# Kernel tuning notes

Measured on AMD Instinct MI355X. Metric: run time of the kernel, lower is better.

## Reference

```python
import jax, jax.numpy as jnp
import numpy as np

DIM = 1024
HEADS = 16
HEAD_DIM = DIM // HEADS


def setup_inputs() -> dict:
    key = jax.random.key(0)
    k_x, k_qkv, k_ow, k_ob = jax.random.split(key, 4)
    x = jax.random.normal(k_x, (2, 2048, DIM), dtype=jnp.float32)
    # nn.Linear(dim, 3*dim, bias=False): weight shape [3*dim, dim], y = x @ W.T
    w_qkv = jax.random.normal(k_qkv, (3 * DIM, DIM), dtype=jnp.float32) * (DIM ** -0.5)
    # nn.Linear(dim, dim) with bias
    w_o = jax.random.normal(k_ow, (DIM, DIM), dtype=jnp.float32) * (DIM ** -0.5)
    b_o = jax.random.normal(k_ob, (DIM,), dtype=jnp.float32) * 0.02
    return {"x": x, "w_qkv": w_qkv, "w_o": w_o, "b_o": b_o}


def reference(x, w_qkv, w_o, b_o):
    b, n, _ = x.shape
    scale = DIM ** -0.5  # NOTE: source scales by full dim, not head dim
    # qkv projection: [b, n, 3*dim]
    qkv = jnp.einsum('bnd,ed->bne', x, w_qkv)
    # 'b n (qkv h d) -> qkv b h n d'
    qkv = qkv.reshape(b, n, 3, HEADS, HEAD_DIM)
    q = jnp.transpose(qkv[:, :, 0], (0, 2, 1, 3))  # [b, h, n, d]
    k = jnp.transpose(qkv[:, :, 1], (0, 2, 1, 3))
    v = jnp.transpose(qkv[:, :, 2], (0, 2, 1, 3))
    scores = jnp.einsum('bhqd,bhkd->bhqk', q, k) * scale  # [b, h, n, n]
    attn = jax.nn.softmax(scores, axis=-1)
    out = jnp.einsum('bhqk,bhkd->bhqd', attn, v)  # [b, h, n, d]
    out = jnp.transpose(out, (0, 2, 1, 3)).reshape(b, n, DIM)  # 'b h n d -> b n (h d)'
    out = jnp.einsum('bnd,ed->bne', out, w_o) + b_o
    return out
```

## Files before the change

### kernel.cpp

```cpp
#include <hip/hip_runtime.h>
#include <stdint.h>


#define DIM 1024
#define SEQ 2048
#define BATCH 2
#define ROWS 4096
#define RSTRIDE 3072

typedef __bf16 bf16_t;
typedef bf16_t bf16x4 __attribute__((ext_vector_type(4)));
typedef bf16_t bf16x8 __attribute__((ext_vector_type(8)));
typedef float f32x4 __attribute__((ext_vector_type(4)));

__device__ __forceinline__ ushort f2bf(float f) {
    uint32_t u;
    __builtin_memcpy(&u, &f, 4);
    uint32_t r = (u + 0x7fffu + ((u >> 16) & 1u)) >> 16;
    return (ushort)r;
}

__device__ __forceinline__ void store_out(ushort* p, float v) { *p = f2bf(v); }
__device__ __forceinline__ void store_out(float* p, float v) { *p = v; }

__device__ __forceinline__ void gl_lds16(const void* g, void* l) {
    __builtin_amdgcn_global_load_lds(
        (const __attribute__((address_space(1))) void*)g,
        (__attribute__((address_space(3))) void*)l, 16, 0, 0);
}

__global__ __launch_bounds__(256) void cvt3_kernel(
    const float* __restrict__ x, const float* __restrict__ wq,
    const float* __restrict__ wo, ushort* __restrict__ dst) {
    size_t i = ((size_t)blockIdx.x * 256 + threadIdx.x) * 8;
    const size_t n_x = (size_t)ROWS * DIM;
    const size_t n_wq = (size_t)3 * DIM * DIM;
    const float* src;
    size_t off;
    if (i < n_x) {
        src = x; off = i;
    } else if (i < n_x + n_wq) {
        src = wq; off = i - n_x;
    } else {
        src = wo; off = i - n_x - n_wq;
    }
    float4 a = *(const float4*)(src + off);
    float4 b = *(const float4*)(src + off + 4);
    uint4 u;
    u.x = (uint)f2bf(a.x) | ((uint)f2bf(a.y) << 16);
    u.y = (uint)f2bf(a.z) | ((uint)f2bf(a.w) << 16);
    u.z = (uint)f2bf(b.x) | ((uint)f2bf(b.y) << 16);
    u.w = (uint)f2bf(b.z) | ((uint)f2bf(b.w) << 16);
    *(uint4*)(dst + i) = u;
}

template <typename OutT, int BN>
__global__ __launch_bounds__(256) void gemm_bt_kernel(
    const ushort* __restrict__ A, const ushort* __restrict__ B,
    const float* __restrict__ bias, OutT* __restrict__ C,
    int M, int N, int K) {
    constexpr int JN = BN / 32;
    __shared__ __align__(16) ushort sA[128 * 64];
    __shared__ __align__(16) ushort sB[BN * 64];

    const int tid = threadIdx.x;
    const int lane = tid & 63, w = tid >> 6;
    const int quad = lane >> 4, l15 = lane & 15;
    const int wm = (w >> 1) * 64, wn = (w & 1) * (BN / 2);
    const int bm = blockIdx.y, bn = blockIdx.x;

    f32x4 acc[4][JN];
#pragma unroll
    for (int i = 0; i < 4; i++)
#pragma unroll
        for (int j = 0; j < JN; j++) acc[i][j] = (f32x4){0.f, 0.f, 0.f, 0.f};

    const ushort* Abase = A + (size_t)(bm * 128) * K;
    const ushort* Bbase = B + (size_t)(bn * BN) * K;
    const int rd = lane >> 3, c8 = lane & 7;
    const int sw = l15 & 7;

    for (int kk = 0; kk < K; kk += 64) {
        __syncthreads();
#pragma unroll
        for (int t = 0; t < 4; t++) {
            int row = w * 32 + t * 8;
            gl_lds16(Abase + (size_t)(row + rd) * K + kk + ((c8 ^ rd) * 8),
                     sA + row * 64);
        }
#pragma unroll
        for (int t = 0; t < BN / 32; t++) {
            int row = w * 8 + t * 32;
            gl_lds16(Bbase + (size_t)(row + rd) * K + kk + ((c8 ^ rd) * 8),
                     sB + row * 64);
        }
        __syncthreads();

#pragma unroll
        for (int kh = 0; kh < 2; kh++) {
            bf16x8 af[4], bfr[JN];
#pragma unroll
            for (int i = 0; i < 4; i++)
                af[i] = *(const bf16x8*)((const bf16_t*)sA +
                        (wm + i * 16 + l15) * 64 + (((kh * 4 + quad) ^ sw) * 8));
#pragma unroll
            for (int j = 0; j < JN; j++)
                bfr[j] = *(const bf16x8*)((const bf16_t*)sB +
                        (wn + j * 16 + l15) * 64 + (((kh * 4 + quad) ^ sw) * 8));
#pragma unroll
            for (int i = 0; i < 4; i++)
#pragma unroll
                for (int j = 0; j < JN; j++)
                    acc[i][j] = __builtin_amdgcn_mfma_f32_16x16x32_bf16(
                        af[i], bfr[j], acc[i][j], 0, 0, 0);
        }
    }

#pragma unroll
    for (int i = 0; i < 4; i++)
#pragma unroll
        for (int j = 0; j < JN; j++) {
            int col = bn * BN + wn + j * 16 + l15;
            float bv = bias ? bias[col] : 0.f;
#pragma unroll
            for (int r = 0; r < 4; r++) {
                int row = bm * 128 + wm + i * 16 + quad * 4 + r;
                store_out(&C[(size_t)row * N + col], acc[i][j][r] + bv);
            }
        }
}

__global__ __launch_bounds__(512) void flash_attn_kernel(
    const ushort* __restrict__ qkv, ushort* __restrict__ out) {
    __shared__ __align__(16) ushort sK[128 * 64];
    __shared__ __align__(16) ushort sVt[64 * 128];
    __shared__ __align__(16) ushort sP[128 * 64];

    const int tid = threadIdx.x;
    const int lane = tid & 63, w = tid >> 6;
    const int quad = lane >> 4, l15 = lane & 15;
    const int sw = l15 & 7;
    const int bh = blockIdx.y, b = bh >> 4, h = bh & 15;
    const int q0 = blockIdx.x * 128;
    const ushort* qkvb = qkv + (size_t)b * SEQ * RSTRIDE + h * 64;

    const ushort* qrow = qkvb + (size_t)(q0 + w * 16 + l15) * RSTRIDE;
    const bf16x8 aq0 = *(const bf16x8*)(qrow + quad * 8);
    const bf16x8 aq1 = *(const bf16x8*)(qrow + 32 + quad * 8);

    const int krow = tid >> 3, kc8 = tid & 7;
    const int kdst = krow * 64 + ((kc8 ^ (krow & 7)) * 8);
    const int vrp = tid & 63, vc = tid >> 6;
    const int vch = vrp >> 2, vlo = vrp & 3;

    uint4 kreg0, kreg1, va, vb;
    {
        const ushort* kp0 = qkvb + (size_t)krow * RSTRIDE + DIM + kc8 * 8;
        kreg0 = *(const uint4*)kp0;
        kreg1 = *(const uint4*)(kp0 + (size_t)64 * RSTRIDE);
        const ushort* v0 = qkvb + (size_t)(2 * vrp) * RSTRIDE + 2 * DIM + vc * 8;
        va = *(const uint4*)v0;
        vb = *(const uint4*)(v0 + RSTRIDE);
    }

    f32x4 l_acc = (f32x4){0.f, 0.f, 0.f, 0.f};
    f32x4 o[4];
#pragma unroll
    for (int j = 0; j < 4; j++) o[j] = (f32x4){0.f, 0.f, 0.f, 0.f};

    bf16x8 vones;
#pragma unroll
    for (int e = 0; e < 8; e++) vones[e] = (bf16_t)1.0f;

    const float c_exp = 0.04508422f;

    uint* vt32 = (uint*)sVt;
    bf16_t* sPb = (bf16_t*)sP;
    const int swp = (l15 & 7) ^ (((l15 >> 3) & 1) << 1);
    for (int kb = 0; kb < SEQ; kb += 128) {
        *(uint4*)(sK + kdst) = kreg0;
        *(uint4*)(sK + 64 * 64 + kdst) = kreg1;
        {
            int base = (vc * 8) * 64 + vlo;
            vt32[base + 0 * 64 + ((vch ^ 0) << 2)] = (va.x & 0xffffu) | (vb.x << 16);
            vt32[base + 1 * 64 + ((vch ^ 1) << 2)] = (va.x >> 16) | (vb.x & 0xffff0000u);
            vt32[base + 2 * 64 + ((vch ^ 2) << 2)] = (va.y & 0xffffu) | (vb.y << 16);
            vt32[base + 3 * 64 + ((vch ^ 3) << 2)] = (va.y >> 16) | (vb.y & 0xffff0000u);
            vt32[base + 4 * 64 + ((vch ^ 4) << 2)] = (va.z & 0xffffu) | (vb.z << 16);
            vt32[base + 5 * 64 + ((vch ^ 5) << 2)] = (va.z >> 16) | (vb.z & 0xffff0000u);
            vt32[base + 6 * 64 + ((vch ^ 6) << 2)] = (va.w & 0xffffu) | (vb.w << 16);
            vt32[base + 7 * 64 + ((vch ^ 7) << 2)] = (va.w >> 16) | (vb.w & 0xffff0000u);
        }
        __syncthreads();

        int nkb = (kb + 128 < SEQ) ? kb + 128 : kb;
        {
            const ushort* kp0 = qkvb + (size_t)(nkb + krow) * RSTRIDE + DIM + kc8 * 8;
            kreg0 = *(const uint4*)kp0;
            kreg1 = *(const uint4*)(kp0 + (size_t)64 * RSTRIDE);
            const ushort* v0 =
                qkvb + (size_t)(nkb + 2 * vrp) * RSTRIDE + 2 * DIM + vc * 8;
            va = *(const uint4*)v0;
            vb = *(const uint4*)(v0 + RSTRIDE);
        }

        f32x4 s[8];
#pragma unroll
        for (int j = 0; j < 8; j++) {
            const ushort* kp = sK + (j * 16 + l15) * 64;
            bf16x8 bk0 = *(const bf16x8*)(kp + ((quad ^ sw) * 8));
            bf16x8 bk1 = *(const bf16x8*)(kp + (((4 | quad) ^ sw) * 8));
            f32x4 z = (f32x4){0.f, 0.f, 0.f, 0.f};
            __builtin_amdgcn_s_setprio(1);
            z = __builtin_amdgcn_mfma_f32_16x16x32_bf16(aq0, bk0, z, 0, 0, 0);
            z = __builtin_amdgcn_mfma_f32_16x16x32_bf16(aq1, bk1, z, 0, 0, 0);
            __builtin_amdgcn_s_setprio(0);
            s[j] = z;
        }

#pragma unroll
        for (int h2 = 0; h2 < 2; h2++) {
#pragma unroll
            for (int j = 0; j < 4; j++)
#pragma unroll
                for (int r = 0; r < 4; r++) {
                    float p = __builtin_amdgcn_exp2f(s[h2 * 4 + j][r] * c_exp);
                    int kr = quad * 4 + r;
                    int row = w * 16 + kr;
                    int ch = j * 2 + (l15 >> 3);
                    int key = (kr & 7) ^ (((kr >> 3) & 1) << 1);
                    sPb[row * 64 + (((ch ^ key) << 3) | (l15 & 7))] =
                        (bf16_t)p;
                }
            const bf16_t* pp = sPb + (w * 16 + l15) * 64;
            bf16x8 pa0 = *(const bf16x8*)(pp + ((quad ^ swp) * 8));
            bf16x8 pa1 = *(const bf16x8*)(pp + (((4 | quad) ^ swp) * 8));
            __builtin_amdgcn_s_setprio(1);
            l_acc = __builtin_amdgcn_mfma_f32_16x16x32_bf16(pa0, vones, l_acc, 0, 0, 0);
            l_acc = __builtin_amdgcn_mfma_f32_16x16x32_bf16(pa1, vones, l_acc, 0, 0, 0);
            __builtin_amdgcn_s_setprio(0);
#pragma unroll
            for (int jd = 0; jd < 4; jd++) {
                const bf16_t* vp = (const bf16_t*)sVt + (jd * 16 + l15) * 128;
                bf16x8 bv0 = *(const bf16x8*)(vp + (((h2 * 8 + quad) ^ sw) * 8));
                bf16x8 bv1 = *(const bf16x8*)(vp + (((h2 * 8 + 4 + quad) ^ sw) * 8));
                __builtin_amdgcn_s_setprio(1);
                o[jd] = __builtin_amdgcn_mfma_f32_16x16x32_bf16(pa0, bv0, o[jd], 0, 0, 0);
                o[jd] = __builtin_amdgcn_mfma_f32_16x16x32_bf16(pa1, bv1, o[jd], 0, 0, 0);
                __builtin_amdgcn_s_setprio(0);
            }
        }
        __syncthreads();
    }

#pragma unroll
    for (int r = 0; r < 4; r++) {
        float inv = 1.f / l_acc[r];
        int qrow_i = q0 + w * 16 + quad * 4 + r;
#pragma unroll
        for (int j = 0; j < 4; j++) {
            out[(size_t)(b * SEQ + qrow_i) * DIM + h * 64 + j * 16 + l15] =
                f2bf(o[j][r] * inv);
        }
    }
}

extern "C" void kernel_launch(void* const* d_in, const int* in_sizes, int n_in,
                              void* d_out, int out_size, void* d_ws, size_t ws_size,
                              hipStream_t stream) {
    const float* x = (const float*)d_in[0];
    const float* w_qkv = (const float*)d_in[1];
    const float* w_o = (const float*)d_in[2];
    const float* b_o = (const float*)d_in[3];
    float* out = (float*)d_out;

    ushort* qkv = (ushort*)d_ws;
    ushort* attn = qkv + (size_t)ROWS * 3 * DIM;
    ushort* xb = attn + (size_t)ROWS * DIM;
    ushort* wqkvb = xb + (size_t)ROWS * DIM;
    ushort* wob = wqkvb + (size_t)3 * DIM * DIM;

    dim3 blk(256);
    cvt3_kernel<<<(ROWS * DIM + 3 * DIM * DIM + DIM * DIM) / 2048, blk, 0,
                  stream>>>(x, w_qkv, w_o, xb);

    gemm_bt_kernel<ushort, 128>
        <<<dim3(3 * DIM / 128, ROWS / 128), blk, 0, stream>>>(
            xb, wqkvb, nullptr, qkv, ROWS, 3 * DIM, DIM);
    flash_attn_kernel<<<dim3(SEQ / 128, BATCH * 16), dim3(512), 0, stream>>>(qkv, attn);
    gemm_bt_kernel<float, 64>
        <<<dim3(DIM / 64, ROWS / 128), blk, 0, stream>>>(
            attn, wob, b_o, out, ROWS, DIM, DIM);
}
```

Baseline: 191.9 us.

## Split attention key block across two wave groups with 64-query tiles

The flash attention block now covers 64 queries instead of 128. Its 8 waves form 4 query groups times 2 key halves: each wave computes scores for 64 of the 128 keys in a tile and accumulates partial O and row sums. At the end the two halves are combined through shared memory. This doubles the grid to raise parallelism and occupancy (launch bounds now request 6 waves per EU), at the cost of loading each K/V tile for twice as many blocks and adding a reduction step.

```diff
diff --git a/kernel.cpp b/kernel.cpp
--- a/kernel.cpp
+++ b/kernel.cpp
@@ -130,7 +130,7 @@
         }
 }
 
-__global__ __launch_bounds__(512) void flash_attn_kernel(
+__global__ __launch_bounds__(512, 6) void flash_attn_kernel(
     const ushort* __restrict__ qkv, ushort* __restrict__ out) {
     __shared__ __align__(16) ushort sK[128 * 64];
     __shared__ __align__(16) ushort sVt[64 * 128];
@@ -138,13 +138,14 @@
 
     const int tid = threadIdx.x;
     const int lane = tid & 63, w = tid >> 6;
+    const int qw = w & 3, kh = w >> 2;
     const int quad = lane >> 4, l15 = lane & 15;
     const int sw = l15 & 7;
     const int bh = blockIdx.y, b = bh >> 4, h = bh & 15;
-    const int q0 = blockIdx.x * 128;
+    const int q0 = blockIdx.x * 64;
     const ushort* qkvb = qkv + (size_t)b * SEQ * RSTRIDE + h * 64;
 
-    const ushort* qrow = qkvb + (size_t)(q0 + w * 16 + l15) * RSTRIDE;
+    const ushort* qrow = qkvb + (size_t)(q0 + qw * 16 + l15) * RSTRIDE;
     const bf16x8 aq0 = *(const bf16x8*)(qrow + quad * 8);
     const bf16x8 aq1 = *(const bf16x8*)(qrow + 32 + quad * 8);
 
@@ -204,10 +205,10 @@
             vb = *(const uint4*)(v0 + RSTRIDE);
         }
 
-        f32x4 s[8];
-#pragma unroll
-        for (int j = 0; j < 8; j++) {
-            const ushort* kp = sK + (j * 16 + l15) * 64;
+        f32x4 s[4];
+#pragma unroll
+        for (int j = 0; j < 4; j++) {
+            const ushort* kp = sK + ((kh * 4 + j) * 16 + l15) * 64;
             bf16x8 bk0 = *(const bf16x8*)(kp + ((quad ^ sw) * 8));
             bf16x8 bk1 = *(const bf16x8*)(kp + (((4 | quad) ^ sw) * 8));
             f32x4 z = (f32x4){0.f, 0.f, 0.f, 0.f};
@@ -219,48 +220,59 @@
         }
 
 #pragma unroll
-        for (int h2 = 0; h2 < 2; h2++) {
-#pragma unroll
-            for (int j = 0; j < 4; j++)
-#pragma unroll
-                for (int r = 0; r < 4; r++) {
-                    float p = __builtin_amdgcn_exp2f(s[h2 * 4 + j][r] * c_exp);
-                    int kr = quad * 4 + r;
-                    int row = w * 16 + kr;
-                    int ch = j * 2 + (l15 >> 3);
-                    int key = (kr & 7) ^ (((kr >> 3) & 1) << 1);
-                    sPb[row * 64 + (((ch ^ key) << 3) | (l15 & 7))] =
-                        (bf16_t)p;
-                }
-            const bf16_t* pp = sPb + (w * 16 + l15) * 64;
-            bf16x8 pa0 = *(const bf16x8*)(pp + ((quad ^ swp) * 8));
-            bf16x8 pa1 = *(const bf16x8*)(pp + (((4 | quad) ^ swp) * 8));
+        for (int j = 0; j < 4; j++)
+#pragma unroll
+            for (int r = 0; r < 4; r++) {
+                float p = __builtin_amdgcn_exp2f(s[j][r] * c_exp);
+                int kr = quad * 4 + r;
+                int row = w * 16 + kr;
+                int ch = j * 2 + (l15 >> 3);
+                int key = (kr & 7) ^ (((kr >> 3) & 1) << 1);
+                sPb[row * 64 + (((ch ^ key) << 3) | (l15 & 7))] = (bf16_t)p;
+            }
+        const bf16_t* pp = sPb + (w * 16 + l15) * 64;
+        bf16x8 pa0 = *(const bf16x8*)(pp + ((quad ^ swp) * 8));
+        bf16x8 pa1 = *(const bf16x8*)(pp + (((4 | quad) ^ swp) * 8));
+        __builtin_amdgcn_s_setprio(1);
+        l_acc = __builtin_amdgcn_mfma_f32_16x16x32_bf16(pa0, vones, l_acc, 0, 0, 0);
+        l_acc = __builtin_amdgcn_mfma_f32_16x16x32_bf16(pa1, vones, l_acc, 0, 0, 0);
+        __builtin_amdgcn_s_setprio(0);
+#pragma unroll
+        for (int jd = 0; jd < 4; jd++) {
+            const bf16_t* vp = (const bf16_t*)sVt + (jd * 16 + l15) * 128;
+            bf16x8 bv0 = *(const bf16x8*)(vp + (((kh * 8 + quad) ^ sw) * 8));
+            bf16x8 bv1 = *(const bf16x8*)(vp + (((kh * 8 + 4 + quad) ^ sw) * 8));
             __builtin_amdgcn_s_setprio(1);
-            l_acc = __builtin_amdgcn_mfma_f32_16x16x32_bf16(pa0, vones, l_acc, 0, 0, 0);
-            l_acc = __builtin_amdgcn_mfma_f32_16x16x32_bf16(pa1, vones, l_acc, 0, 0, 0);
+            o[jd] = __builtin_amdgcn_mfma_f32_16x16x32_bf16(pa0, bv0, o[jd], 0, 0, 0);
+            o[jd] = __builtin_amdgcn_mfma_f32_16x16x32_bf16(pa1, bv1, o[jd], 0, 0, 0);
             __builtin_amdgcn_s_setprio(0);
+        }
+        __syncthreads();
+    }
+
+    float* sO = (float*)sVt;
+    float* sL = (float*)sK;
+    if (kh == 1) {
+#pragma unroll
+        for (int jd = 0; jd < 4; jd++)
+            *(f32x4*)(sO + ((qw * 4 + jd) * 64 + lane) * 4) = o[jd];
+        *(f32x4*)(sL + (qw * 64 + lane) * 4) = l_acc;
+    }
+    __syncthreads();
+    if (kh == 0) {
+        l_acc += *(const f32x4*)(sL + (qw * 64 + lane) * 4);
+#pragma unroll
+        for (int jd = 0; jd < 4; jd++)
+            o[jd] += *(const f32x4*)(sO + ((qw * 4 + jd) * 64 + lane) * 4);
+#pragma unroll
+        for (int r = 0; r < 4; r++) {
+            float inv = 1.f / l_acc[r];
+            int qrow_i = q0 + qw * 16 + quad * 4 + r;
 #pragma unroll
             for (int jd = 0; jd < 4; jd++) {
-                const bf16_t* vp = (const bf16_t*)sVt + (jd * 16 + l15) * 128;
-                bf16x8 bv0 = *(const bf16x8*)(vp + (((h2 * 8 + quad) ^ sw) * 8));
-                bf16x8 bv1 = *(const bf16x8*)(vp + (((h2 * 8 + 4 + quad) ^ sw) * 8));
-                __builtin_amdgcn_s_setprio(1);
-                o[jd] = __builtin_amdgcn_mfma_f32_16x16x32_bf16(pa0, bv0, o[jd], 0, 0, 0);
-                o[jd] = __builtin_amdgcn_mfma_f32_16x16x32_bf16(pa1, bv1, o[jd], 0, 0, 0);
-                __builtin_amdgcn_s_setprio(0);
+                out[(size_t)(b * SEQ + qrow_i) * DIM + h * 64 + jd * 16 + l15] =
+                    f2bf(o[jd][r] * inv);
             }
-        }
-        __syncthreads();
-    }
-
-#pragma unroll
-    for (int r = 0; r < 4; r++) {
-        float inv = 1.f / l_acc[r];
-        int qrow_i = q0 + w * 16 + quad * 4 + r;
-#pragma unroll
-        for (int j = 0; j < 4; j++) {
-            out[(size_t)(b * SEQ + qrow_i) * DIM + h * 64 + j * 16 + l15] =
-                f2bf(o[j][r] * inv);
         }
     }
 }
@@ -287,7 +299,7 @@
     gemm_bt_kernel<ushort, 128>
         <<<dim3(3 * DIM / 128, ROWS / 128), blk, 0, stream>>>(
             xb, wqkvb, nullptr, qkv, ROWS, 3 * DIM, DIM);
-    flash_attn_kernel<<<dim3(SEQ / 128, BATCH * 16), dim3(512), 0, stream>>>(qkv, attn);
+    flash_attn_kernel<<<dim3(SEQ / 64, BATCH * 16), dim3(512), 0, stream>>>(qkv, attn);
     gemm_bt_kernel<float, 64>
         <<<dim3(DIM / 64, ROWS / 128), blk, 0, stream>>>(
             attn, wob, b_o, out, ROWS, DIM, DIM);
```

Result: slower. 337.6 us (+76.0%).

## Keep attention probabilities in registers via transposed QK^T and 16x16x16 MFMA

Applied to the files above, without the earlier changes.

Swaps the MFMA operands for QK^T so each lane's score fragment already matches the A-operand layout of a 16x16x16 bf16 MFMA. The P tile no longer round-trips through shared memory. The row-sum and PV products then use the K=16 instruction directly on register data, and the sP buffer is removed. This cuts LDS writes/reads and LDS footprint (launch bounds now request 4 waves per SIMD occupancy hint), at the cost of using twice as many smaller-K MFMAs with narrower V loads.

```diff
diff --git a/kernel.cpp b/kernel.cpp
--- a/kernel.cpp
+++ b/kernel.cpp
@@ -12,6 +12,7 @@
 typedef bf16_t bf16x4 __attribute__((ext_vector_type(4)));
 typedef bf16_t bf16x8 __attribute__((ext_vector_type(8)));
 typedef float f32x4 __attribute__((ext_vector_type(4)));
+typedef short s16x4 __attribute__((ext_vector_type(4)));
 
 __device__ __forceinline__ ushort f2bf(float f) {
     uint32_t u;
@@ -130,16 +131,16 @@
         }
 }
 
-__global__ __launch_bounds__(512) void flash_attn_kernel(
+__global__ __launch_bounds__(512, 4) void flash_attn_kernel(
     const ushort* __restrict__ qkv, ushort* __restrict__ out) {
     __shared__ __align__(16) ushort sK[128 * 64];
     __shared__ __align__(16) ushort sVt[64 * 128];
-    __shared__ __align__(16) ushort sP[128 * 64];
 
     const int tid = threadIdx.x;
     const int lane = tid & 63, w = tid >> 6;
     const int quad = lane >> 4, l15 = lane & 15;
     const int sw = l15 & 7;
+    const int qh = quad >> 1, q1 = quad & 1;
     const int bh = blockIdx.y, b = bh >> 4, h = bh & 15;
     const int q0 = blockIdx.x * 128;
     const ushort* qkvb = qkv + (size_t)b * SEQ * RSTRIDE + h * 64;
@@ -168,15 +169,13 @@
 #pragma unroll
     for (int j = 0; j < 4; j++) o[j] = (f32x4){0.f, 0.f, 0.f, 0.f};
 
-    bf16x8 vones;
-#pragma unroll
-    for (int e = 0; e < 8; e++) vones[e] = (bf16_t)1.0f;
+    s16x4 vones;
+#pragma unroll
+    for (int e = 0; e < 4; e++) vones[e] = (short)0x3F80;
 
     const float c_exp = 0.04508422f;
 
     uint* vt32 = (uint*)sVt;
-    bf16_t* sPb = (bf16_t*)sP;
-    const int swp = (l15 & 7) ^ (((l15 >> 3) & 1) << 1);
     for (int kb = 0; kb < SEQ; kb += 128) {
         *(uint4*)(sK + kdst) = kreg0;
         *(uint4*)(sK + 64 * 64 + kdst) = kreg1;
@@ -212,43 +211,41 @@
             bf16x8 bk1 = *(const bf16x8*)(kp + (((4 | quad) ^ sw) * 8));
             f32x4 z = (f32x4){0.f, 0.f, 0.f, 0.f};
             __builtin_amdgcn_s_setprio(1);
-            z = __builtin_amdgcn_mfma_f32_16x16x32_bf16(aq0, bk0, z, 0, 0, 0);
-            z = __builtin_amdgcn_mfma_f32_16x16x32_bf16(aq1, bk1, z, 0, 0, 0);
+            z = __builtin_amdgcn_mfma_f32_16x16x32_bf16(bk0, aq0, z, 0, 0, 0);
+            z = __builtin_amdgcn_mfma_f32_16x16x32_bf16(bk1, aq1, z, 0, 0, 0);
             __builtin_amdgcn_s_setprio(0);
             s[j] = z;
         }
 
-#pragma unroll
-        for (int h2 = 0; h2 < 2; h2++) {
-#pragma unroll
-            for (int j = 0; j < 4; j++)
-#pragma unroll
-                for (int r = 0; r < 4; r++) {
-                    float p = __builtin_amdgcn_exp2f(s[h2 * 4 + j][r] * c_exp);
-                    int kr = quad * 4 + r;
-                    int row = w * 16 + kr;
-                    int ch = j * 2 + (l15 >> 3);
-                    int key = (kr & 7) ^ (((kr >> 3) & 1) << 1);
-                    sPb[row * 64 + (((ch ^ key) << 3) | (l15 & 7))] =
-                        (bf16_t)p;
-                }
-            const bf16_t* pp = sPb + (w * 16 + l15) * 64;
-            bf16x8 pa0 = *(const bf16x8*)(pp + ((quad ^ swp) * 8));
-            bf16x8 pa1 = *(const bf16x8*)(pp + (((4 | quad) ^ swp) * 8));
+        s16x4 pa[8];
+#pragma unroll
+        for (int j = 0; j < 8; j++) {
+            bf16x4 t;
+#pragma unroll
+            for (int r = 0; r < 4; r++)
+                t[r] = (bf16_t)__builtin_amdgcn_exp2f(s[j][r] * c_exp);
+            pa[j] = __builtin_bit_cast(s16x4, t);
+        }
+
+        __builtin_amdgcn_s_setprio(1);
+#pragma unroll
+        for (int j = 0; j < 8; j++)
+            l_acc = __builtin_amdgcn_mfma_f32_16x16x16bf16_1k(
+                pa[j], vones, l_acc, 0, 0, 0);
+        __builtin_amdgcn_s_setprio(0);
+
+#pragma unroll
+        for (int jd = 0; jd < 4; jd++) {
+            const bf16_t* vp = (const bf16_t*)sVt + (jd * 16 + l15) * 128;
             __builtin_amdgcn_s_setprio(1);
-            l_acc = __builtin_amdgcn_mfma_f32_16x16x32_bf16(pa0, vones, l_acc, 0, 0, 0);
-            l_acc = __builtin_amdgcn_mfma_f32_16x16x32_bf16(pa1, vones, l_acc, 0, 0, 0);
+#pragma unroll
+            for (int j = 0; j < 8; j++) {
+                int ch = 2 * j + qh;
+                bf16x4 bv = *(const bf16x4*)(vp + ((ch ^ sw) * 8 + q1 * 4));
+                o[jd] = __builtin_amdgcn_mfma_f32_16x16x16bf16_1k(
+                    pa[j], __builtin_bit_cast(s16x4, bv), o[jd], 0, 0, 0);
+            }
             __builtin_amdgcn_s_setprio(0);
-#pragma unroll
-            for (int jd = 0; jd < 4; jd++) {
-                const bf16_t* vp = (const bf16_t*)sVt + (jd * 16 + l15) * 128;
-                bf16x8 bv0 = *(const bf16x8*)(vp + (((h2 * 8 + quad) ^ sw) * 8));
-                bf16x8 bv1 = *(const bf16x8*)(vp + (((h2 * 8 + 4 + quad) ^ sw) * 8));
-                __builtin_amdgcn_s_setprio(1);
-                o[jd] = __builtin_amdgcn_mfma_f32_16x16x32_bf16(pa0, bv0, o[jd], 0, 0, 0);
-                o[jd] = __builtin_amdgcn_mfma_f32_16x16x32_bf16(pa1, bv1, o[jd], 0, 0, 0);
-                __builtin_amdgcn_s_setprio(0);
-            }
         }
         __syncthreads();
     }
```

Result: faster. 187.6 us (-2.2%).
